# Performance work log

Hardware: AMD Instinct MI355X
Metric: run time of the kernel (lower is better)

Reference implementation:

```python
import jax, jax.numpy as jnp
import numpy as np


def setup_inputs() -> dict:
    key = jax.random.key(0)
    k1, k2, k3 = jax.random.split(key, 3)
    B, N, T_BG, T_IN = 32, 64, 512, 256
    surv_steps = jax.random.uniform(k1, (B, N, T_BG), dtype=jnp.float32)
    time_bg = jax.random.uniform(k2, (T_BG,), dtype=jnp.float32)
    time_in = jax.random.uniform(k3, (T_IN,), dtype=jnp.float32)
    bandwidth = jnp.ones((1,), dtype=jnp.float32)  # learned parameter
    return {
        "surv_steps": surv_steps,
        "time_bg": time_bg,
        "time_in": time_in,
        "bandwidth": bandwidth,
        "single_time": 0,
    }


def reference(surv_steps, time_bg, time_in, bandwidth, single_time):
    # bandwidth.clamp_min(1e-6)
    b = jnp.maximum(bandwidth, 1e-6)  # [1]
    # pairwise abs time difference: [T_in, T_bg]
    t_metric = jnp.abs(time_bg[None, :] - time_in[:, None])
    # softmin(x) == softmax(-x), over the background-time axis
    t_weights = jax.nn.softmax(-(b * t_metric), axis=-1)  # [T_in, T_bg]
    if single_time:
        # t_weights -> [T_in, 1, T_bg], surv_hist = surv_steps broadcast over middle dim
        proba = jnp.sum(t_weights[:, None, :] * surv_steps, axis=-1)
    else:
        # t_weights -> [1,1,T_in,T_bg], surv_hist = surv_steps[..., None, :]
        # sum over T_bg == contraction: [B,N,T_bg] x [T_in,T_bg] -> [B,N,T_in]
        proba = jnp.einsum("bnt,it->bni", surv_steps, t_weights)
    return proba
```

## Files before the change

kernel.cpp:

```cpp
#include <hip/hip_runtime.h>
#include <math.h>

constexpr int TBG = 512;
constexpr int TIN = 256;
constexpr int M   = 2048;

constexpr int BM = 32;
constexpr int BN = 64;
constexpr int BK = 128;
constexpr int EPAD = 8;
constexpr int APAD = 8;

typedef __attribute__((ext_vector_type(8))) short bf16x8;
typedef __attribute__((ext_vector_type(4))) float f32x4;

__device__ __forceinline__ unsigned short f2bf(float f) {
    unsigned u = __float_as_uint(f);
    u += 0x7FFFu + ((u >> 16) & 1u);
    return (unsigned short)(u >> 16);
}

__global__ __launch_bounds__(512, 2) void fused_kernel(
    const float* __restrict__ A,
    const float* __restrict__ time_bg,
    const float* __restrict__ time_in,
    const float* __restrict__ bandwidth,
    float* __restrict__ C)
{
    __shared__ unsigned short Es[BN][TBG + EPAD];
    __shared__ unsigned short As[BM][BK + APAD];
    __shared__ float Pt[TBG];
    __shared__ float Pti[TBG];
    __shared__ float red[BN][8];
    __shared__ float invS[BN];

    const int tid = threadIdx.x;
    const int i0  = blockIdx.x * BN;
    const int m0  = blockIdx.y * BM;
    const float b = fmaxf(bandwidth[0], 1e-6f);

    {
        const float t = time_bg[tid];
        Pt[tid]  = __expf(b * t);
        Pti[tid] = __expf(-b * t);
    }
    __syncthreads();

    {
        const int   i   = tid >> 3;
        const int   o   = tid & 7;
        const float ti  = time_in[i0 + i];
        const float qi  = __expf(-b * ti);
        const float qii = __expf(b * ti);
        float s = 0.f;
        #pragma unroll
        for (int j0 = 0; j0 < 64; j0 += 8) {
            const int t0 = o * 64 + j0;
            const float4 p0  = *(const float4*)&Pt[t0];
            const float4 p1  = *(const float4*)&Pt[t0 + 4];
            const float4 q0  = *(const float4*)&Pti[t0];
            const float4 q1  = *(const float4*)&Pti[t0 + 4];
            float e[8];
            e[0] = fminf(p0.x * qi, q0.x * qii);
            e[1] = fminf(p0.y * qi, q0.y * qii);
            e[2] = fminf(p0.z * qi, q0.z * qii);
            e[3] = fminf(p0.w * qi, q0.w * qii);
            e[4] = fminf(p1.x * qi, q1.x * qii);
            e[5] = fminf(p1.y * qi, q1.y * qii);
            e[6] = fminf(p1.z * qi, q1.z * qii);
            e[7] = fminf(p1.w * qi, q1.w * qii);
            bf16x8 pk;
            #pragma unroll
            for (int j = 0; j < 8; ++j) {
                s += e[j];
                pk[j] = (short)f2bf(e[j]);
            }
            *(bf16x8*)&Es[i][t0] = pk;
        }
        red[i][o] = s;
    }
    __syncthreads();

    if (tid < BN) {
        float s = 0.f;
        #pragma unroll
        for (int o = 0; o < 8; ++o) s += red[tid][o];
        invS[tid] = 1.0f / s;
    }

    const int w    = tid >> 6;
    const int mt   = w >> 2;
    const int ig   = w & 3;
    const int lane = tid & 63;
    const int col  = lane & 15;
    const int quad = lane >> 4;

    const int ar = tid >> 4;
    const int ac = (tid & 15) << 3;

    f32x4 acc = {0.f, 0.f, 0.f, 0.f};

    for (int k0 = 0; k0 < TBG; k0 += BK) {
        {
            const float* ap = A + (m0 + ar) * TBG + k0 + ac;
            const float4 x = *(const float4*)ap;
            const float4 y = *(const float4*)(ap + 4);
            bf16x8 pk;
            pk[0] = (short)f2bf(x.x); pk[1] = (short)f2bf(x.y);
            pk[2] = (short)f2bf(x.z); pk[3] = (short)f2bf(x.w);
            pk[4] = (short)f2bf(y.x); pk[5] = (short)f2bf(y.y);
            pk[6] = (short)f2bf(y.z); pk[7] = (short)f2bf(y.w);
            *(bf16x8*)&As[ar][ac] = pk;
        }
        __syncthreads();

        #pragma unroll
        for (int s = 0; s < 4; ++s) {
            const int ks = s * 32 + quad * 8;
            const bf16x8 bfr = *(const bf16x8*)&Es[ig * 16 + col][k0 + ks];
            const bf16x8 afr = *(const bf16x8*)&As[mt * 16 + col][ks];
            acc = __builtin_amdgcn_mfma_f32_16x16x32_bf16(afr, bfr, acc, 0, 0, 0);
        }
        __syncthreads();
    }

    const float isv = invS[ig * 16 + col];
    #pragma unroll
    for (int v = 0; v < 4; ++v) {
        const int m = m0 + mt * 16 + quad * 4 + v;
        C[m * TIN + i0 + ig * 16 + col] = acc[v] * isv;
    }
}

extern "C" void kernel_launch(void* const* d_in, const int* in_sizes, int n_in,
                              void* d_out, int out_size, void* d_ws, size_t ws_size,
                              hipStream_t stream)
{
    const float* surv      = (const float*)d_in[0];
    const float* time_bg   = (const float*)d_in[1];
    const float* time_in   = (const float*)d_in[2];
    const float* bandwidth = (const float*)d_in[3];

    float* out = (float*)d_out;

    fused_kernel<<<dim3(TIN / BN, M / BM), dim3(512), 0, stream>>>(
        surv, time_bg, time_in, bandwidth, out);
}
```

Baseline: 70.62 us.

## Load A fragments directly into registers with prefetch, drop LDS staging and barriers

The A operand no longer goes through a shared-memory tile with two barriers per K step. Each wave loads its MFMA fragment straight from global memory into registers, prefetching four steps ahead, and the first loads are issued before the softmax weight table is built so that latency overlaps. The float-to-bf16 conversion now uses the packed hardware instruction v_cvt_pk_bf16_f32. The weight-table work is remapped to lane×wave, and each thread computes its own normalizer from red[], which removes a serial reduction and a barrier. The cost is that waves sharing a row tile now reload A redundantly from global memory or cache instead of sharing it through LDS, and register pressure rises.

After: 70.44 us. Within noise of the previous version (-0.3%).

```diff
diff --git a/kernel.cpp b/kernel.cpp
--- a/kernel.cpp
+++ b/kernel.cpp
@@ -7,17 +7,15 @@
 
 constexpr int BM = 32;
 constexpr int BN = 64;
-constexpr int BK = 128;
 constexpr int EPAD = 8;
-constexpr int APAD = 8;
 
 typedef __attribute__((ext_vector_type(8))) short bf16x8;
 typedef __attribute__((ext_vector_type(4))) float f32x4;
 
-__device__ __forceinline__ unsigned short f2bf(float f) {
-    unsigned u = __float_as_uint(f);
-    u += 0x7FFFu + ((u >> 16) & 1u);
-    return (unsigned short)(u >> 16);
+__device__ __forceinline__ unsigned cvt_pk_bf16(float lo, float hi) {
+    unsigned r;
+    asm("v_cvt_pk_bf16_f32 %0, %1, %2" : "=v"(r) : "v"(lo), "v"(hi));
+    return r;
 }
 
 __global__ __launch_bounds__(512, 2) void fused_kernel(
@@ -28,16 +26,23 @@
     float* __restrict__ C)
 {
     __shared__ unsigned short Es[BN][TBG + EPAD];
-    __shared__ unsigned short As[BM][BK + APAD];
     __shared__ float Pt[TBG];
     __shared__ float Pti[TBG];
     __shared__ float red[BN][8];
-    __shared__ float invS[BN];
 
     const int tid = threadIdx.x;
     const int i0  = blockIdx.x * BN;
     const int m0  = blockIdx.y * BM;
     const float b = fmaxf(bandwidth[0], 1e-6f);
+
+    const int w    = tid >> 6;
+    const int mt   = w >> 2;
+    const int ig   = w & 3;
+    const int lane = tid & 63;
+    const int col  = lane & 15;
+    const int quad = lane >> 4;
+
+    const float* arow = A + (m0 + mt * 16 + col) * TBG + quad * 8;
 
     {
         const float t = time_bg[tid];
@@ -46,85 +51,70 @@
     }
     __syncthreads();
 
+    float4 pf[4][2];
+    #pragma unroll
+    for (int s = 0; s < 4; ++s) {
+        pf[s][0] = *(const float4*)(arow + s * 32);
+        pf[s][1] = *(const float4*)(arow + s * 32 + 4);
+    }
+
     {
-        const int   i   = tid >> 3;
-        const int   o   = tid & 7;
-        const float ti  = time_in[i0 + i];
+        const int   t0  = w * 64;
+        const float ti  = time_in[i0 + lane];
         const float qi  = __expf(-b * ti);
         const float qii = __expf(b * ti);
         float s = 0.f;
         #pragma unroll
         for (int j0 = 0; j0 < 64; j0 += 8) {
-            const int t0 = o * 64 + j0;
-            const float4 p0  = *(const float4*)&Pt[t0];
-            const float4 p1  = *(const float4*)&Pt[t0 + 4];
-            const float4 q0  = *(const float4*)&Pti[t0];
-            const float4 q1  = *(const float4*)&Pti[t0 + 4];
-            float e[8];
-            e[0] = fminf(p0.x * qi, q0.x * qii);
-            e[1] = fminf(p0.y * qi, q0.y * qii);
-            e[2] = fminf(p0.z * qi, q0.z * qii);
-            e[3] = fminf(p0.w * qi, q0.w * qii);
-            e[4] = fminf(p1.x * qi, q1.x * qii);
-            e[5] = fminf(p1.y * qi, q1.y * qii);
-            e[6] = fminf(p1.z * qi, q1.z * qii);
-            e[7] = fminf(p1.w * qi, q1.w * qii);
-            bf16x8 pk;
-            #pragma unroll
-            for (int j = 0; j < 8; ++j) {
-                s += e[j];
-                pk[j] = (short)f2bf(e[j]);
-            }
-            *(bf16x8*)&Es[i][t0] = pk;
+            const float4 p0 = *(const float4*)&Pt[t0 + j0];
+            const float4 p1 = *(const float4*)&Pt[t0 + j0 + 4];
+            const float4 q0 = *(const float4*)&Pti[t0 + j0];
+            const float4 q1 = *(const float4*)&Pti[t0 + j0 + 4];
+            const float e0 = fminf(p0.x * qi, q0.x * qii);
+            const float e1 = fminf(p0.y * qi, q0.y * qii);
+            const float e2 = fminf(p0.z * qi, q0.z * qii);
+            const float e3 = fminf(p0.w * qi, q0.w * qii);
+            const float e4 = fminf(p1.x * qi, q1.x * qii);
+            const float e5 = fminf(p1.y * qi, q1.y * qii);
+            const float e6 = fminf(p1.z * qi, q1.z * qii);
+            const float e7 = fminf(p1.w * qi, q1.w * qii);
+            s += ((e0 + e1) + (e2 + e3)) + ((e4 + e5) + (e6 + e7));
+            union { bf16x8 v; unsigned u[4]; } pk;
+            pk.u[0] = cvt_pk_bf16(e0, e1);
+            pk.u[1] = cvt_pk_bf16(e2, e3);
+            pk.u[2] = cvt_pk_bf16(e4, e5);
+            pk.u[3] = cvt_pk_bf16(e6, e7);
+            *(bf16x8*)&Es[lane][t0 + j0] = pk.v;
         }
-        red[i][o] = s;
+        red[lane][w] = s;
     }
     __syncthreads();
 
-    if (tid < BN) {
-        float s = 0.f;
-        #pragma unroll
-        for (int o = 0; o < 8; ++o) s += red[tid][o];
-        invS[tid] = 1.0f / s;
+    const unsigned short* erow = &Es[ig * 16 + col][quad * 8];
+    f32x4 acc = {0.f, 0.f, 0.f, 0.f};
+    #pragma unroll
+    for (int s = 0; s < 16; ++s) {
+        const float4 x = pf[s & 3][0];
+        const float4 y = pf[s & 3][1];
+        if (s + 4 < 16) {
+            pf[s & 3][0] = *(const float4*)(arow + (s + 4) * 32);
+            pf[s & 3][1] = *(const float4*)(arow + (s + 4) * 32 + 4);
+        }
+        union { bf16x8 v; unsigned u[4]; } af;
+        af.u[0] = cvt_pk_bf16(x.x, x.y);
+        af.u[1] = cvt_pk_bf16(x.z, x.w);
+        af.u[2] = cvt_pk_bf16(y.x, y.y);
+        af.u[3] = cvt_pk_bf16(y.z, y.w);
+        const bf16x8 bfr = *(const bf16x8*)(erow + s * 32);
+        acc = __builtin_amdgcn_mfma_f32_16x16x32_bf16(af.v, bfr, acc, 0, 0, 0);
     }
 
-    const int w    = tid >> 6;
-    const int mt   = w >> 2;
-    const int ig   = w & 3;
-    const int lane = tid & 63;
-    const int col  = lane & 15;
-    const int quad = lane >> 4;
-
-    const int ar = tid >> 4;
-    const int ac = (tid & 15) << 3;
-
-    f32x4 acc = {0.f, 0.f, 0.f, 0.f};
-
-    for (int k0 = 0; k0 < TBG; k0 += BK) {
-        {
-            const float* ap = A + (m0 + ar) * TBG + k0 + ac;
-            const float4 x = *(const float4*)ap;
-            const float4 y = *(const float4*)(ap + 4);
-            bf16x8 pk;
-            pk[0] = (short)f2bf(x.x); pk[1] = (short)f2bf(x.y);
-            pk[2] = (short)f2bf(x.z); pk[3] = (short)f2bf(x.w);
-            pk[4] = (short)f2bf(y.x); pk[5] = (short)f2bf(y.y);
-            pk[6] = (short)f2bf(y.z); pk[7] = (short)f2bf(y.w);
-            *(bf16x8*)&As[ar][ac] = pk;
-        }
-        __syncthreads();
-
-        #pragma unroll
-        for (int s = 0; s < 4; ++s) {
-            const int ks = s * 32 + quad * 8;
-            const bf16x8 bfr = *(const bf16x8*)&Es[ig * 16 + col][k0 + ks];
-            const bf16x8 afr = *(const bf16x8*)&As[mt * 16 + col][ks];
-            acc = __builtin_amdgcn_mfma_f32_16x16x32_bf16(afr, bfr, acc, 0, 0, 0);
-        }
-        __syncthreads();
-    }
-
-    const float isv = invS[ig * 16 + col];
+    const int ei = ig * 16 + col;
+    const float4 r0 = *(const float4*)&red[ei][0];
+    const float4 r1 = *(const float4*)&red[ei][4];
+    const float sum = ((r0.x + r0.y) + (r0.z + r0.w)) +
+                      ((r1.x + r1.y) + (r1.z + r1.w));
+    const float isv = 1.0f / sum;
     #pragma unroll
     for (int v = 0; v < 4; ++v) {
         const int m = m0 + mt * 16 + quad * 4 + v;
```
